# Performance work log

Measured on AMD Instinct MI355X. Metric: run time of the kernel, lower is better.

## Reference

```python
import jax, jax.numpy as jnp
import numpy as np

IMG = 224; P = 16; C = 3
G = IMG // P; N = G * G            # 14, 196 patches
DIM = 768; DEPTH = 6; HEADS = 12; DH = 64; MLP = 3072
INNER = HEADS * DH                  # 768
PD = C * P * P                      # 768 patch_dim
B = 32


def _coords():
    m, n = np.meshgrid(np.arange(G), np.arange(G))
    return jnp.asarray(np.stack((m, n), axis=-1).reshape(-1, 2), jnp.float32)  # (N,2)


def _ln(x, g, b, eps=1e-5):
    mu = jnp.mean(x, -1, keepdims=True)
    var = jnp.mean((x - mu) ** 2, -1, keepdims=True)
    return (x - mu) * jax.lax.rsqrt(var + eps) * g + b


def setup_inputs() -> dict:
    key = jax.random.key(0)
    ks = jax.random.split(key, 16)
    s = 0.02
    inp = {
        "img": jax.random.normal(ks[0], (B, C, IMG, IMG), jnp.float32),
        "noise_token": jnp.zeros((1,), jnp.float32),
        "A_noise": jax.random.normal(ks[1], (B, 2, 2), jnp.float32),
        "b_noise": jax.random.normal(ks[2], (B, 2), jnp.float32),
        "A_mean": jnp.eye(2, dtype=jnp.float32),
        "b_mean": jnp.zeros((2,), jnp.float32),
        "A_std": jnp.zeros((2, 2), jnp.float32),   # variance_init=0.0
        "b_std": jnp.zeros((2,), jnp.float32),
        "band_width": jnp.asarray(1.0, jnp.float32),
        "Wp": jax.random.normal(ks[3], (PD, DIM), jnp.float32) * s,
        "bp": jnp.zeros((DIM,), jnp.float32),
        "ln1_g": jnp.ones((DEPTH, DIM), jnp.float32),
        "ln1_b": jnp.zeros((DEPTH, DIM), jnp.float32),
        "Wqkv": jax.random.normal(ks[4], (DEPTH, DIM, 3 * INNER), jnp.float32) * s,
        "Wout": jax.random.normal(ks[5], (DEPTH, INNER, DIM), jnp.float32) * s,
        "bout": jnp.zeros((DEPTH, DIM), jnp.float32),
        "ln2_g": jnp.ones((DEPTH, DIM), jnp.float32),
        "ln2_b": jnp.zeros((DEPTH, DIM), jnp.float32),
        "Wff1": jax.random.normal(ks[6], (DEPTH, DIM, MLP), jnp.float32) * s,
        "bff1": jnp.zeros((DEPTH, MLP), jnp.float32),
        "Wff2": jax.random.normal(ks[7], (DEPTH, MLP, DIM), jnp.float32) * s,
        "bff2": jnp.zeros((DEPTH, DIM), jnp.float32),
        "Wep": jax.random.normal(ks[8], (DIM, PD), jnp.float32) * s,
        "bep": jnp.zeros((PD,), jnp.float32),
    }
    return inp


def reference(img, noise_token, A_noise, b_noise, A_mean, b_mean, A_std, b_std,
              band_width, Wp, bp, ln1_g, ln1_b, Wqkv, Wout, bout,
              ln2_g, ln2_b, Wff1, bff1, Wff2, bff2, Wep, bep):
    del noise_token  # deleted in the original forward
    b = img.shape[0]
    X = _coords()  # (N,2) base patch grid coords, non-trainable buffer
    # patchify: b c (h p1) (w p2) -> b (h w) (p1 p2 c)
    x = img.reshape(b, C, G, P, G, P).transpose(0, 2, 4, 3, 5, 1).reshape(b, N, PD)
    x = x @ Wp + bp
    # stochastic affine transform of coordinates
    A = A_mean + jax.nn.softplus(A_std) * A_noise          # (b,2,2)
    bt = b_mean + jax.nn.softplus(b_std) * b_noise         # (b,2)
    Xt = jnp.einsum('pd,bdo->bpo', X, A) + bt[:, None, :]  # (b,N,2)
    # RBF attention scores: dots[b,i,j] = -||Xt[b,j] - X[i]||^2 / band_width
    diff = Xt[:, None, :, :] - X[None, :, None, :]         # (b,N,N,2)
    dots = -jnp.sum(diff ** 2, axis=-1) / band_width       # (b,N,N)
    attn = jax.nn.softmax(dots, axis=-1)                   # same for all heads/layers
    for l in range(DEPTH):
        y = _ln(x, ln1_g[l], ln1_b[l])
        qkv = y @ Wqkv[l]                                  # q,k unused (pos_only=True)
        v = qkv[..., 2 * INNER:].reshape(b, N, HEADS, DH).transpose(0, 2, 1, 3)
        o = jnp.einsum('bij,bhjd->bhid', attn, v)
        o = o.transpose(0, 2, 1, 3).reshape(b, N, INNER)
        x = o @ Wout[l] + bout[l]                          # NOTE: no residual on attention (matches source)
        h = _ln(x, ln2_g[l], ln2_b[l])
        h = jax.nn.gelu(h @ Wff1[l] + bff1[l], approximate=False) @ Wff2[l] + bff2[l]
        x = x + h
    x = x @ Wep + bep
    # un-patchify: b (h w) (p1 p2 c) -> b c (h p1) (w p2)
    out = x.reshape(b, G, G, P, P, C).transpose(0, 5, 1, 3, 2, 4).reshape(b, C, IMG, IMG)
    return out
```

## Files before the change

### kernel.cpp

```cpp
#include <hip/hip_runtime.h>
#include <hip/hip_bf16.h>
#include <math.h>

#define NTOK 196
#define KPAD 224
#define BATCH 32
#define ROWS (BATCH * NTOK)
#define DIMC 768
#define MLPD 3072

typedef __hip_bfloat16 bf16;
typedef short bf16x8 __attribute__((ext_vector_type(8)));
typedef float f32x4 __attribute__((ext_vector_type(4)));

__device__ __forceinline__ void gload16(const void* g, void* l) {
    __builtin_amdgcn_global_load_lds(
        (__attribute__((address_space(1))) void*)const_cast<void*>(g),
        (__attribute__((address_space(3))) void*)l, 16, 0, 0);
}

__device__ __forceinline__ float softplus_f(float x) {
    return fmaxf(x, 0.f) + log1pf(expf(-fabsf(x)));
}
__device__ __forceinline__ float gelu_f(float x) {
    return 0.5f * x * (1.f + erff(x * 0.70710678118654752f));
}
__device__ __forceinline__ float to_f(float x) { return x; }
__device__ __forceinline__ float to_f(bf16 x) { return __bfloat162float(x); }

__global__ __launch_bounds__(64) void attn_kernel(
    const float* __restrict__ A_noise, const float* __restrict__ b_noise,
    const float* __restrict__ A_mean,  const float* __restrict__ b_mean,
    const float* __restrict__ A_std,   const float* __restrict__ b_std,
    const float* __restrict__ bwp, bf16* __restrict__ attn)
{
    int bi = blockIdx.x;
    int b = bi / NTOK, i = bi % NTOK;
    int lane = threadIdx.x;
    float A00 = A_mean[0] + softplus_f(A_std[0]) * A_noise[b * 4 + 0];
    float A01 = A_mean[1] + softplus_f(A_std[1]) * A_noise[b * 4 + 1];
    float A10 = A_mean[2] + softplus_f(A_std[2]) * A_noise[b * 4 + 2];
    float A11 = A_mean[3] + softplus_f(A_std[3]) * A_noise[b * 4 + 3];
    float bt0 = b_mean[0] + softplus_f(b_std[0]) * b_noise[b * 2 + 0];
    float bt1 = b_mean[1] + softplus_f(b_std[1]) * b_noise[b * 2 + 1];
    float inv_bw = 1.f / bwp[0];
    float Xi0 = (float)(i % 14), Xi1 = (float)(i / 14);
    float d[4];
    float mx = -1e30f;
    #pragma unroll
    for (int r = 0; r < 4; ++r) {
        int j = lane + r * 64;
        if (j < NTOK) {
            float Xj0 = (float)(j % 14), Xj1 = (float)(j / 14);
            float t0 = Xj0 * A00 + Xj1 * A10 + bt0 - Xi0;
            float t1 = Xj0 * A01 + Xj1 * A11 + bt1 - Xi1;
            d[r] = -(t0 * t0 + t1 * t1) * inv_bw;
            mx = fmaxf(mx, d[r]);
        } else d[r] = -1e30f;
    }
    for (int off = 1; off < 64; off <<= 1) mx = fmaxf(mx, __shfl_xor(mx, off));
    float e[4]; float s = 0.f;
    #pragma unroll
    for (int r = 0; r < 4; ++r) {
        int j = lane + r * 64;
        e[r] = (j < NTOK) ? expf(d[r] - mx) : 0.f;
        s += e[r];
    }
    for (int off = 1; off < 64; off <<= 1) s += __shfl_xor(s, off);
    float inv = 1.f / s;
    bf16* row = attn + (long)bi * KPAD;
    #pragma unroll
    for (int r = 0; r < 4; ++r) {
        int j = lane + r * 64;
        if (j < KPAD) row[j] = __float2bfloat16(j < NTOK ? e[r] * inv : 0.f);
    }
}

__global__ __launch_bounds__(256) void patchify_kernel(
    const float* __restrict__ img, bf16* __restrict__ Xp)
{
    long idx = (long)blockIdx.x * 256 + threadIdx.x;
    if (idx >= (long)ROWS * DIMC) return;
    int pd = (int)(idx % DIMC); long r = idx / DIMC;
    int n = (int)(r % NTOK); int b = (int)(r / NTOK);
    int c = pd % 3; int pp = pd / 3; int p2 = pp % 16; int p1 = pp / 16;
    int gw = n % 14, gh = n / 14;
    int h = gh * 16 + p1, w = gw * 16 + p2;
    Xp[idx] = __float2bfloat16(img[(((long)b * 3 + c) * 224 + h) * 224 + w]);
}

__global__ __launch_bounds__(256) void unpatchify_kernel(
    const float* __restrict__ xe, float* __restrict__ out)
{
    long idx = (long)blockIdx.x * 256 + threadIdx.x;
    if (idx >= (long)BATCH * 3 * 224 * 224) return;
    int w = (int)(idx % 224); long r = idx / 224;
    int h = (int)(r % 224); r /= 224;
    int c = (int)(r % 3); int b = (int)(r / 3);
    int gh = h / 16, p1 = h % 16, gw = w / 16, p2 = w % 16;
    int n = gh * 14 + gw;
    int pd = (p1 * 16 + p2) * 3 + c;
    out[idx] = xe[((long)b * NTOK + n) * DIMC + pd];
}

__global__ __launch_bounds__(256) void ln_kernel(
    const float* __restrict__ x, const float* __restrict__ g,
    const float* __restrict__ bb, bf16* __restrict__ y)
{
    int row = blockIdx.x;
    const float* xr = x + (long)row * DIMC;
    bf16* yr = y + (long)row * DIMC;
    int t = threadIdx.x;
    float v0 = xr[t], v1 = xr[t + 256], v2 = xr[t + 512];
    float s = v0 + v1 + v2;
    float s2 = v0 * v0 + v1 * v1 + v2 * v2;
    for (int off = 32; off; off >>= 1) { s += __shfl_down(s, off); s2 += __shfl_down(s2, off); }
    __shared__ float ps[4], ps2[4];
    if ((t & 63) == 0) { ps[t >> 6] = s; ps2[t >> 6] = s2; }
    __syncthreads();
    float S = ps[0] + ps[1] + ps[2] + ps[3];
    float S2 = ps2[0] + ps2[1] + ps2[2] + ps2[3];
    float mean = S * (1.f / DIMC);
    float var = S2 * (1.f / DIMC) - mean * mean;
    float rs = rsqrtf(var + 1e-5f);
    yr[t]       = __float2bfloat16((v0 - mean) * rs * g[t]       + bb[t]);
    yr[t + 256] = __float2bfloat16((v1 - mean) * rs * g[t + 256] + bb[t + 256]);
    yr[t + 512] = __float2bfloat16((v2 - mean) * rs * g[t + 512] + bb[t + 512]);
}

template<int MODE>
__global__ __launch_bounds__(256) void combine_ln(
    const float* __restrict__ P0, const float* __restrict__ P1,
    const float* __restrict__ bias, const float* __restrict__ x,
    const float* __restrict__ g, const float* __restrict__ bb,
    bf16* __restrict__ zb)
{
    int row = blockIdx.x;
    const float* xr = x + (long)row * DIMC;
    const float* p0 = P0 + (long)row * DIMC;
    const float* p1 = P1 + (long)row * DIMC;
    bf16* zr = zb + (long)row * DIMC;
    int t = threadIdx.x;
    float v0 = xr[t]       + p0[t]       + p1[t]       + bias[t];
    float v1 = xr[t + 256] + p0[t + 256] + p1[t + 256] + bias[t + 256];
    float v2 = xr[t + 512] + p0[t + 512] + p1[t + 512] + bias[t + 512];
    if (MODE == 1) {
        zr[t]       = __float2bfloat16(v0);
        zr[t + 256] = __float2bfloat16(v1);
        zr[t + 512] = __float2bfloat16(v2);
        return;
    }
    float s = v0 + v1 + v2;
    float s2 = v0 * v0 + v1 * v1 + v2 * v2;
    for (int off = 32; off; off >>= 1) { s += __shfl_down(s, off); s2 += __shfl_down(s2, off); }
    __shared__ float ps[4], ps2[4];
    if ((t & 63) == 0) { ps[t >> 6] = s; ps2[t >> 6] = s2; }
    __syncthreads();
    float S = ps[0] + ps[1] + ps[2] + ps[3];
    float S2 = ps2[0] + ps2[1] + ps2[2] + ps2[3];
    float mean = S * (1.f / DIMC);
    float var = S2 * (1.f / DIMC) - mean * mean;
    float rs = rsqrtf(var + 1e-5f);
    zr[t]       = __float2bfloat16((v0 - mean) * rs * g[t]       + bb[t]);
    zr[t + 256] = __float2bfloat16((v1 - mean) * rs * g[t + 256] + bb[t + 256]);
    zr[t + 512] = __float2bfloat16((v2 - mean) * rs * g[t + 512] + bb[t + 512]);
}

template<typename TIN>
__global__ __launch_bounds__(256) void transpose_cvt(
    const TIN* __restrict__ in, bf16* __restrict__ out,
    int R, int C, int ldin, int ldout, int Rpad, long sIn, long sOut)
{
    __shared__ float tile[32][33];
    in  += (long)blockIdx.z * sIn;
    out += (long)blockIdx.z * sOut;
    int c0 = blockIdx.x * 32, r0 = blockIdx.y * 32;
    int tx = threadIdx.x & 31, ty = threadIdx.x >> 5;
    #pragma unroll
    for (int i = 0; i < 32; i += 8) {
        int r = r0 + ty + i, c = c0 + tx;
        float v = 0.f;
        if (r < R && c < C) v = to_f(in[(long)r * ldin + c]);
        tile[ty + i][tx] = v;
    }
    __syncthreads();
    #pragma unroll
    for (int i = 0; i < 32; i += 8) {
        int c = c0 + ty + i, r = r0 + tx;
        if (c < C && r < Rpad) out[(long)c * ldout + r] = __float2bfloat16(tile[tx][ty + i]);
    }
}

__global__ __launch_bounds__(256) void cvt_wv_kernel(const float* __restrict__ Wqkv,
                                                     bf16* __restrict__ out)
{
    long i = (long)blockIdx.x * 256 + threadIdx.x;
    if (i >= 6L * 768 * 768) return;
    int c = (int)(i % 768); long rl = i / 768;
    int r = (int)(rl % 768); int l = (int)(rl / 768);
    out[i] = __float2bfloat16(Wqkv[((long)l * 768 + r) * 2304 + 1536 + c]);
}

template<int BN, int ACT, int ACCUM, int OUTF32, int GUARDM>
__global__ __launch_bounds__(256) void gemm_bf16(
    const bf16* __restrict__ A, const bf16* __restrict__ Bt,
    const float* __restrict__ bias, void* __restrict__ Cv,
    int M, int K, int lda, int ldb, int ldc,
    long sA, long sB, long sC)
{
    constexpr int FN = BN / 32;
    constexpr int LPT = 2 + BN / 64;
    constexpr int BSTRIDE = BN * 32;
    constexpr int SMEM = (BN == 128) ? 49152 : 36864;
    __shared__ __align__(16) char smem[SMEM];
    bf16* As = (bf16*)smem;
    bf16* Bs = (bf16*)(smem + 3 * 8192);
    A  += (long)blockIdx.z * sA;
    Bt += (long)blockIdx.z * sB;
    const int nwg = gridDim.x * gridDim.y;
    const int id = blockIdx.x + gridDim.x * blockIdx.y;
    const int q8 = nwg >> 3, r8 = nwg & 7;
    const int xcd = id & 7, jj = id >> 3;
    const int v = (xcd < r8 ? xcd * (q8 + 1) : r8 * (q8 + 1) + (xcd - r8) * q8) + jj;
    const int bx = v % gridDim.x, by = v / gridDim.x;
    const int m0 = by * 128, n0 = bx * BN;
    const int t = threadIdx.x, wave = t >> 6, lane = t & 63;
    const int lrow = t >> 2;
    const int lcol = ((t & 3) ^ ((lrow >> 1) & 3)) * 8;
    const bf16* ag = A  + (long)(m0 + lrow) * lda + lcol;
    const bf16* bg = Bt + (long)(n0 + lrow) * ldb + lcol;
    const int fr = lane & 15, kq = lane >> 4;
    const int swz = (fr >> 1) & 3;
    const int wr = wave >> 1, wc = wave & 1;
    f32x4 acc[4][FN];
    #pragma unroll
    for (int m = 0; m < 4; ++m)
        #pragma unroll
        for (int n = 0; n < FN; ++n) acc[m][n] = (f32x4){0.f, 0.f, 0.f, 0.f};

    auto stage = [&](int kt, int bufi) {
        const int k0 = kt << 5;
        bf16* ab = As + bufi * 4096 + wave * 512;
        bf16* bb = Bs + bufi * BSTRIDE + wave * 512;
        gload16(ag + k0, ab);
        gload16(ag + 64 * (long)lda + k0, ab + 2048);
        gload16(bg + k0, bb);
        if constexpr (BN == 128) gload16(bg + 64 * (long)ldb + k0, bb + 2048);
    };
    auto compute = [&](int bufi) {
        const bf16* as = As + bufi * 4096;
        const bf16* bs = Bs + bufi * BSTRIDE;
        bf16x8 af[4], bfv[FN];
        #pragma unroll
        for (int m = 0; m < 4; ++m)
            af[m] = *(const bf16x8*)&as[(wr * 64 + m * 16 + fr) * 32 + ((kq ^ swz) << 3)];
        #pragma unroll
        for (int n = 0; n < FN; ++n)
            bfv[n] = *(const bf16x8*)&bs[(wc * (BN / 2) + n * 16 + fr) * 32 + ((kq ^ swz) << 3)];
        __builtin_amdgcn_s_setprio(1);
        #pragma unroll
        for (int m = 0; m < 4; ++m)
            #pragma unroll
            for (int n = 0; n < FN; ++n)
                acc[m][n] = __builtin_amdgcn_mfma_f32_16x16x32_bf16(af[m], bfv[n], acc[m][n], 0, 0, 0);
        __builtin_amdgcn_s_setprio(0);
    };

    const int nt = K >> 5;
    stage(0, 0);
    stage(1, 1);
    int cur = 0, pf = 2;
    for (int it = 0; it < nt - 1; ++it) {
        asm volatile("s_waitcnt vmcnt(%0)" :: "n"(LPT) : "memory");
        __builtin_amdgcn_s_barrier();
        __builtin_amdgcn_sched_barrier(0);
        if (it + 2 < nt) stage(it + 2, pf);
        compute(cur);
        cur = (cur == 2) ? 0 : cur + 1;
        pf  = (pf  == 2) ? 0 : pf + 1;
    }
    asm volatile("s_waitcnt vmcnt(0)" ::: "memory");
    __builtin_amdgcn_s_barrier();
    __builtin_amdgcn_sched_barrier(0);
    compute(cur);
    __syncthreads();

    const int rbase = kq * 4;
    if constexpr (OUTF32) {
        static_assert(BN == 64, "f32 epilogue assumes BN=64");
        float* Cs = (float*)smem;
        #pragma unroll
        for (int n = 0; n < FN; ++n) {
            int lc = wc * (BN / 2) + n * 16 + fr;
            float bi = bias ? bias[n0 + lc] : 0.f;
            #pragma unroll
            for (int m = 0; m < 4; ++m)
                #pragma unroll
                for (int r = 0; r < 4; ++r) {
                    int lr = wr * 64 + m * 16 + rbase + r;
                    float vv = acc[m][n][r] + bi;
                    if (ACT) vv = gelu_f(vv);
                    Cs[lr * BN + lc] = vv;
                }
        }
        __syncthreads();
        float* Cp = (float*)Cv + (long)blockIdx.z * sC;
        #pragma unroll
        for (int i = 0; i < (128 * BN) / (256 * 4); ++i) {
            int chunk = i * 256 + t;
            int row = chunk / (BN / 4), c4 = (chunk % (BN / 4)) * 4;
            int gm = m0 + row;
            if (GUARDM && gm >= M) continue;
            float4 v4 = *(const float4*)&Cs[row * BN + c4];
            float* p = Cp + (long)gm * ldc + n0 + c4;
            if (ACCUM) {
                float4 o4 = *(const float4*)p;
                v4.x += o4.x; v4.y += o4.y; v4.z += o4.z; v4.w += o4.w;
            }
            *(float4*)p = v4;
        }
    } else {
        bf16* Cs = (bf16*)smem;
        #pragma unroll
        for (int n = 0; n < FN; ++n) {
            int lc = wc * (BN / 2) + n * 16 + fr;
            float bi = bias ? bias[n0 + lc] : 0.f;
            #pragma unroll
            for (int m = 0; m < 4; ++m)
                #pragma unroll
                for (int r = 0; r < 4; ++r) {
                    int lr = wr * 64 + m * 16 + rbase + r;
                    float vv = acc[m][n][r] + bi;
                    if (ACT) vv = gelu_f(vv);
                    Cs[lr * BN + lc] = __float2bfloat16(vv);
                }
        }
        __syncthreads();
        bf16* Cp = (bf16*)Cv + (long)blockIdx.z * sC;
        #pragma unroll
        for (int i = 0; i < (128 * BN) / (256 * 8); ++i) {
            int chunk = i * 256 + t;
            int row = chunk / (BN / 8), c8 = (chunk % (BN / 8)) * 8;
            int gm = m0 + row;
            if (GUARDM && gm >= M) continue;
            *(bf16x8*)(Cp + (long)gm * ldc + n0 + c8) = *(const bf16x8*)&Cs[row * BN + c8];
        }
    }
}

extern "C" void kernel_launch(void* const* d_in, const int* in_sizes, int n_in,
                              void* d_out, int out_size, void* d_ws, size_t ws_size,
                              hipStream_t stream) {
    const float* img     = (const float*)d_in[0];
    const float* A_noise = (const float*)d_in[2];
    const float* b_noise = (const float*)d_in[3];
    const float* A_mean  = (const float*)d_in[4];
    const float* b_mean  = (const float*)d_in[5];
    const float* A_std   = (const float*)d_in[6];
    const float* b_std   = (const float*)d_in[7];
    const float* band_w  = (const float*)d_in[8];
    const float* Wp      = (const float*)d_in[9];
    const float* bp      = (const float*)d_in[10];
    const float* ln1_g   = (const float*)d_in[11];
    const float* ln1_b   = (const float*)d_in[12];
    const float* Wqkv    = (const float*)d_in[13];
    const float* Wout    = (const float*)d_in[14];
    const float* bout    = (const float*)d_in[15];
    const float* ln2_g   = (const float*)d_in[16];
    const float* ln2_b   = (const float*)d_in[17];
    const float* Wff1    = (const float*)d_in[18];
    const float* bff1    = (const float*)d_in[19];
    const float* Wff2    = (const float*)d_in[20];
    const float* bff2    = (const float*)d_in[21];
    const float* Wep     = (const float*)d_in[22];
    const float* bep     = (const float*)d_in[23];
    float* out = (float*)d_out;

    char* w = (char*)d_ws;
    bf16* WpT  = (bf16*)w; w += 768L * 768 * 2;
    bf16* WepT = (bf16*)w; w += 768L * 768 * 2;
    bf16* WvoT = (bf16*)w; w += 6L * 768 * 768 * 2;
    bf16* Wf1T = (bf16*)w; w += 6L * 3072 * 768 * 2;
    bf16* Wf2T = (bf16*)w; w += 6L * 768 * 3072 * 2;
    bf16* attnb = (bf16*)w; w += (long)(ROWS + 64) * KPAD * 2;
    bf16* Xpb  = (bf16*)w; w += (long)ROWS * DIMC * 2;
    bf16* yb   = (bf16*)w; w += (long)ROWS * DIMC * 2;
    bf16* yTb  = (bf16*)w; w += (long)BATCH * DIMC * KPAD * 2;
    bf16* ya   = (bf16*)w; w += (long)ROWS * DIMC * 2;
    bf16* h1b  = (bf16*)w; w += (long)ROWS * MLPD * 2;
    float* x   = (float*)w; w += (long)ROWS * DIMC * 4;
    float* P0 = (float*)Xpb;
    float* P1 = P0 + (long)ROWS * DIMC;
    bf16* WoT = h1b;
    bf16* Wvb = h1b + 6L * 768 * 768;
    bf16* zb  = h1b;
    float* xe = (float*)((char*)h1b + (long)ROWS * DIMC * 2);

    transpose_cvt<float><<<dim3(24, 24, 1), 256, 0, stream>>>(Wp,  WpT,  768, 768, 768, 768, 768, 0, 0);
    transpose_cvt<float><<<dim3(24, 24, 1), 256, 0, stream>>>(Wep, WepT, 768, 768, 768, 768, 768, 0, 0);
    transpose_cvt<float><<<dim3(24, 24, 6), 256, 0, stream>>>(Wout, WoT, 768, 768, 768, 768, 768,
                                                              768L * 768, 768L * 768);
    cvt_wv_kernel<<<(int)((6L * 768 * 768 + 255) / 256), 256, 0, stream>>>(Wqkv, Wvb);
    transpose_cvt<float><<<dim3(96, 24, 6), 256, 0, stream>>>(Wff1, Wf1T, 768, 3072, 3072, 768, 768,
                                                              768L * 3072, 3072L * 768);
    transpose_cvt<float><<<dim3(24, 96, 6), 256, 0, stream>>>(Wff2, Wf2T, 3072, 768, 768, 3072, 3072,
                                                              3072L * 768, 768L * 3072);
    gemm_bf16<64, 0, 0, 0, 0><<<dim3(12, 6, 6), 256, 0, stream>>>(
        WoT, Wvb, nullptr, WvoT, 768, 768, 768, 768, 768,
        768L * 768, 768L * 768, 768L * 768);

    attn_kernel<<<ROWS, 64, 0, stream>>>(A_noise, b_noise, A_mean, b_mean, A_std, b_std, band_w, attnb);

    patchify_kernel<<<(ROWS * DIMC + 255) / 256, 256, 0, stream>>>(img, Xpb);
    gemm_bf16<64, 0, 0, 1, 0><<<dim3(12, 49, 1), 256, 0, stream>>>(
        Xpb, WpT, bp, x, ROWS, 768, 768, 768, 768, 0, 0, 0);
    ln_kernel<<<ROWS, 256, 0, stream>>>(x, ln1_g, ln1_b, zb);

    for (int l = 0; l < 6; ++l) {
        transpose_cvt<bf16><<<dim3(24, 7, 32), 256, 0, stream>>>(
            zb, yTb, NTOK, 768, 768, KPAD, KPAD, (long)NTOK * 768, (long)768 * KPAD);
        gemm_bf16<64, 0, 0, 0, 1><<<dim3(12, 2, BATCH), 256, 0, stream>>>(
            attnb, yTb, nullptr, ya, NTOK, KPAD, KPAD, KPAD, 768,
            (long)NTOK * KPAD, (long)768 * KPAD, (long)NTOK * 768);
        gemm_bf16<64, 0, 0, 1, 0><<<dim3(12, 49, 1), 256, 0, stream>>>(
            ya, WvoT + (long)l * 768 * 768, bout + l * 768, x, ROWS, 768, 768, 768, 768, 0, 0, 0);
        ln_kernel<<<ROWS, 256, 0, stream>>>(x, ln2_g + l * 768, ln2_b + l * 768, yb);
        gemm_bf16<64, 1, 0, 0, 0><<<dim3(48, 49, 1), 256, 0, stream>>>(
            yb, Wf1T + (long)l * 3072 * 768, bff1 + l * 3072, h1b, ROWS, 768, 768, 768, 3072, 0, 0, 0);
        gemm_bf16<64, 0, 0, 1, 0><<<dim3(12, 49, 2), 256, 0, stream>>>(
            h1b, Wf2T + (long)l * 768 * 3072, nullptr, P0,
            ROWS, 1536, 3072, 3072, 768, 1536, 1536, (long)ROWS * DIMC);
        if (l < 5)
            combine_ln<0><<<ROWS, 256, 0, stream>>>(P0, P1, bff2 + l * 768, x,
                ln1_g + (l + 1) * 768, ln1_b + (l + 1) * 768, zb);
        else
            combine_ln<1><<<ROWS, 256, 0, stream>>>(P0, P1, bff2 + l * 768, x,
                ln1_g, ln1_b, zb);
    }

    gemm_bf16<64, 0, 0, 1, 0><<<dim3(12, 49, 1), 256, 0, stream>>>(
        zb, WepT, bep, xe, ROWS, 768, 768, 768, 768, 0, 0, 0);
    unpatchify_kernel<<<(BATCH * 3 * 224 * 224 + 255) / 256, 256, 0, stream>>>(xe, out);
}
```

Baseline: 1.180 ms.

## Switch GEMM LDS pipeline from triple to double buffering

Replaces the three-stage LDS ring with a two-buffer ping-pong that prefetches one k-tile ahead. Each iteration now adds an extra barrier before staging so the buffer being overwritten is no longer in use. The LDS footprint is resized to the larger of the main-loop and epilogue needs, which lowers shared memory per block and may raise occupancy. In exchange, prefetch depth shrinks and synchronisation per iteration increases, so global-load latency is less hidden.

```diff
diff --git a/kernel.cpp b/kernel.cpp
--- a/kernel.cpp
+++ b/kernel.cpp
@@ -210,11 +210,14 @@
 {
     constexpr int FN = BN / 32;
     constexpr int LPT = 2 + BN / 64;
-    constexpr int BSTRIDE = BN * 32;
-    constexpr int SMEM = (BN == 128) ? 49152 : 36864;
+    constexpr int ABUF = 128 * 32;
+    constexpr int BBUF = BN * 32;
+    constexpr int SMEM_MAIN = 2 * (ABUF + BBUF) * 2;
+    constexpr int SMEM_EPI  = OUTF32 ? (128 * BN * 4) : (128 * BN * 2);
+    constexpr int SMEM = SMEM_MAIN > SMEM_EPI ? SMEM_MAIN : SMEM_EPI;
     __shared__ __align__(16) char smem[SMEM];
     bf16* As = (bf16*)smem;
-    bf16* Bs = (bf16*)(smem + 3 * 8192);
+    bf16* Bs = (bf16*)(smem + 2 * ABUF * 2);
     A  += (long)blockIdx.z * sA;
     Bt += (long)blockIdx.z * sB;
     const int nwg = gridDim.x * gridDim.y;
@@ -240,16 +243,16 @@
 
     auto stage = [&](int kt, int bufi) {
         const int k0 = kt << 5;
-        bf16* ab = As + bufi * 4096 + wave * 512;
-        bf16* bb = Bs + bufi * BSTRIDE + wave * 512;
+        bf16* ab = As + bufi * ABUF + wave * 512;
+        bf16* bb = Bs + bufi * BBUF + wave * 512;
         gload16(ag + k0, ab);
         gload16(ag + 64 * (long)lda + k0, ab + 2048);
         gload16(bg + k0, bb);
         if constexpr (BN == 128) gload16(bg + 64 * (long)ldb + k0, bb + 2048);
     };
     auto compute = [&](int bufi) {
-        const bf16* as = As + bufi * 4096;
-        const bf16* bs = Bs + bufi * BSTRIDE;
+        const bf16* as = As + bufi * ABUF;
+        const bf16* bs = Bs + bufi * BBUF;
         bf16x8 af[4], bfv[FN];
         #pragma unroll
         for (int m = 0; m < 4; ++m)
@@ -268,21 +271,19 @@
 
     const int nt = K >> 5;
     stage(0, 0);
-    stage(1, 1);
-    int cur = 0, pf = 2;
-    for (int it = 0; it < nt - 1; ++it) {
-        asm volatile("s_waitcnt vmcnt(%0)" :: "n"(LPT) : "memory");
+    for (int it = 0; it < nt; ++it) {
+        const int cb = it & 1;
+        if (it) __builtin_amdgcn_s_barrier();
+        if (it + 1 < nt) {
+            stage(it + 1, cb ^ 1);
+            asm volatile("s_waitcnt vmcnt(%0)" :: "n"(LPT) : "memory");
+        } else {
+            asm volatile("s_waitcnt vmcnt(0)" ::: "memory");
+        }
         __builtin_amdgcn_s_barrier();
         __builtin_amdgcn_sched_barrier(0);
-        if (it + 2 < nt) stage(it + 2, pf);
-        compute(cur);
-        cur = (cur == 2) ? 0 : cur + 1;
-        pf  = (pf  == 2) ? 0 : pf + 1;
-    }
-    asm volatile("s_waitcnt vmcnt(0)" ::: "memory");
-    __builtin_amdgcn_s_barrier();
-    __builtin_amdgcn_sched_barrier(0);
-    compute(cur);
+        compute(cb);
+    }
     __syncthreads();
 
     const int rbase = kq * 4;
```

Measured after the change: 1.190 ms. No clear change (+0.8%).
